# Optimization experiments

Measured on AMD Instinct MI355X. Metric: run time of the kernel, lower is better.

Reference implementation:

```python
import jax, jax.numpy as jnp
import numpy as np

EMBED = 128
HEADS = 8
DH = EMBED // HEADS
FFN_HIDDEN = 512
B, N = 16, 256


def layer_norm(x, g, b, eps=1e-5):
    mu = jnp.mean(x, axis=-1, keepdims=True)
    var = jnp.var(x, axis=-1, keepdims=True)
    return (x - mu) * jax.lax.rsqrt(var + eps) * g + b


def setup_inputs() -> dict:
    key = jax.random.key(0)
    ks = jax.random.split(key, 12)
    s = 1.0 / np.sqrt(EMBED)
    inp = {
        "x": jax.random.normal(ks[0], (B, N, EMBED), jnp.float32),
        "global_rel_pe": jax.random.normal(ks[1], (B, N, N, EMBED), jnp.float32),
        "attn_mask": jnp.zeros((B, N, N), jnp.float32),
        "ln1_g": jnp.ones((EMBED,), jnp.float32),
        "ln1_b": jnp.zeros((EMBED,), jnp.float32),
        "Wq": jax.random.normal(ks[2], (EMBED, EMBED), jnp.float32) * s,
        "bq": jnp.zeros((EMBED,), jnp.float32),
        "Wk": jax.random.normal(ks[3], (EMBED, EMBED), jnp.float32) * s,
        "bk": jnp.zeros((EMBED,), jnp.float32),
        "Wv": jax.random.normal(ks[4], (EMBED, EMBED), jnp.float32) * s,
        "bv": jnp.zeros((EMBED,), jnp.float32),
        "Wo": jax.random.normal(ks[5], (EMBED, EMBED), jnp.float32) * s,
        "bo": jnp.zeros((EMBED,), jnp.float32),
        "ln2_g": jnp.ones((EMBED,), jnp.float32),
        "ln2_b": jnp.zeros((EMBED,), jnp.float32),
        "W1": jax.random.normal(ks[6], (EMBED, FFN_HIDDEN), jnp.float32) * s,
        "b1": jnp.zeros((FFN_HIDDEN,), jnp.float32),
        "W2": jax.random.normal(ks[7], (FFN_HIDDEN, EMBED), jnp.float32) * (1.0 / np.sqrt(FFN_HIDDEN)),
        "b2": jnp.zeros((EMBED,), jnp.float32),
    }
    return inp


def reference(x, global_rel_pe, attn_mask, ln1_g, ln1_b, Wq, bq, Wk, bk, Wv, bv,
              Wo, bo, ln2_g, ln2_b, W1, b1, W2, b2):
    b, n, d = x.shape
    xn = layer_norm(x, ln1_g, ln1_b)
    q = (xn @ Wq + bq).reshape(b, n, HEADS, DH)
    k = (xn @ Wk + bk).reshape(b, n, HEADS, DH)
    v = (xn @ Wv + bv).reshape(b, n, HEADS, DH)
    pe = global_rel_pe.reshape(b, n, n, HEADS, DH)
    # content scores + rel-pos scores: key augmented per-pair by rel_pe
    content = jnp.einsum("bihd,bjhd->bhij", q, k)
    pos = jnp.einsum("bihd,bijhd->bhij", q, pe)
    scores = (content + pos) * (1.0 / np.sqrt(DH)) + attn_mask[:, None]
    attn = jax.nn.softmax(scores, axis=-1)  # [B,H,N,N]
    ctx = jnp.einsum("bhij,bjhd->bihd", attn, v).reshape(b, n, d)
    attn_out = ctx @ Wo + bo
    x = x + attn_out
    xn = layer_norm(x, ln2_g, ln2_b)
    ffn = jax.nn.relu(xn @ W1 + b1) @ W2 + b2
    return x + ffn
```

## Files before the change

### kernel.cpp

```cpp
#include <hip/hip_runtime.h>
#include <hip/hip_bf16.h>
#include <hip/hip_fp16.h>

#define EMBED 128
#define HEADS 8
#define DH 16
#define FFN 512
#define BB 16
#define NN 256

typedef float floatx4 __attribute__((ext_vector_type(4)));

__global__ __launch_bounds__(128) void ln1_qkv_kernel(
    const float* __restrict__ x,
    const float* __restrict__ ln1_g, const float* __restrict__ ln1_b,
    const float* __restrict__ Wq, const float* __restrict__ bq,
    const float* __restrict__ Wk, const float* __restrict__ bk,
    const float* __restrict__ Wv, const float* __restrict__ bv,
    float* __restrict__ q, float* __restrict__ k, float* __restrict__ v)
{
    const int row0 = blockIdx.x * 8;
    const int t    = threadIdx.x;
    const int wv_  = t >> 6;
    const int l64  = t & 63;

    __shared__ float xn[8][EMBED];

    #pragma unroll
    for (int rr = 0; rr < 4; ++rr) {
        const int r = wv_ * 4 + rr;
        const float v0 = x[(size_t)(row0 + r) * EMBED + l64];
        const float v1 = x[(size_t)(row0 + r) * EMBED + 64 + l64];
        float s  = v0 + v1;
        float sq = v0 * v0 + v1 * v1;
        #pragma unroll
        for (int off = 32; off >= 1; off >>= 1) {
            s  += __shfl_xor(s, off);
            sq += __shfl_xor(sq, off);
        }
        const float mu  = s * (1.0f / EMBED);
        const float var = sq * (1.0f / EMBED) - mu * mu;
        const float rs  = rsqrtf(var + 1e-5f);
        xn[r][l64]      = (v0 - mu) * rs * ln1_g[l64]      + ln1_b[l64];
        xn[r][l64 + 64] = (v1 - mu) * rs * ln1_g[l64 + 64] + ln1_b[l64 + 64];
    }
    __syncthreads();

    const int e = t;
    float aq[8], ak[8], av[8];
    const float bqe = bq[e], bke = bk[e], bve = bv[e];
    #pragma unroll
    for (int r = 0; r < 8; ++r) { aq[r] = bqe; ak[r] = bke; av[r] = bve; }

    #pragma unroll 4
    for (int c = 0; c < EMBED; ++c) {
        const float wq = Wq[c * EMBED + e];
        const float wk = Wk[c * EMBED + e];
        const float wv2 = Wv[c * EMBED + e];
        #pragma unroll
        for (int r = 0; r < 8; ++r) {
            const float xc = xn[r][c];
            aq[r] += xc * wq;
            ak[r] += xc * wk;
            av[r] += xc * wv2;
        }
    }
    #pragma unroll
    for (int r = 0; r < 8; ++r) {
        const size_t o = (size_t)(row0 + r) * EMBED + e;
        q[o] = aq[r]; k[o] = ak[r]; v[o] = av[r];
    }
}

__global__ __launch_bounds__(256) void scores_pv_kernel(
    const float* __restrict__ pe,
    const float* __restrict__ mask,
    const float* __restrict__ q, const float* __restrict__ k,
    const float* __restrict__ v,
    const float* __restrict__ x,
    const float* __restrict__ Wo, const float* __restrict__ bo,
    const float* __restrict__ ln2_g, const float* __restrict__ ln2_b,
    float* __restrict__ x2g, float* __restrict__ xn2g)
{
    const int bid  = blockIdx.x;
    const int blk  = (bid & 7) * 128 + (bid >> 3);
    const int row0 = blk * 4;
    const int bb   = row0 >> 8;
    const int t    = threadIdx.x;

    __shared__ __half sc[4][HEADS][264];
    __shared__ float msk[4][NN];
    __shared__ float red4[4][4][EMBED];
    __shared__ float ctx[4][EMBED];
    __shared__ float wred[2][4][EMBED];
    __shared__ float x2s[4][EMBED];

    const int g = t >> 5;
    const int l = t & 31;

    #pragma unroll
    for (int r = 0; r < 4; ++r)
        msk[r][t] = mask[(size_t)(row0 + r) * NN + t];

    floatx4 q4[4];
    #pragma unroll
    for (int r = 0; r < 4; ++r)
        q4[r] = *reinterpret_cast<const floatx4*>(q + (size_t)(row0 + r) * EMBED + 4 * l);

    const size_t pe_base = (size_t)row0 * NN * EMBED;
    const size_t k_row   = (size_t)bb * NN * EMBED;
    const int rot = blk & 31;

    #pragma unroll 4
    for (int jt0 = 0; jt0 < 32; ++jt0) {
        const int jt = (jt0 + rot) & 31;
        const int j  = jt * 8 + g;
        const floatx4 k4 = *reinterpret_cast<const floatx4*>(k + k_row + (size_t)j * EMBED + 4 * l);
        #pragma unroll
        for (int r = 0; r < 4; ++r) {
            const floatx4 p4 = __builtin_nontemporal_load(
                reinterpret_cast<const floatx4*>(pe + pe_base + ((size_t)r * NN + j) * EMBED + 4 * l));
            const floatx4 sum = k4 + p4;
            float s = q4[r].x * sum.x + q4[r].y * sum.y + q4[r].z * sum.z + q4[r].w * sum.w;
            s += __shfl_xor(s, 1);
            s += __shfl_xor(s, 2);
            if ((l & 3) == 0) sc[r][l >> 2][j] = __float2half(s * 0.25f);
        }
    }
    __syncthreads();

    #pragma unroll
    for (int r = 0; r < 4; ++r) {
        float vals[8];
        float m = -1e30f;
        #pragma unroll
        for (int rr = 0; rr < 8; ++rr) {
            vals[rr] = __half2float(sc[r][g][l + 32 * rr]) + msk[r][l + 32 * rr];
            m = fmaxf(m, vals[rr]);
        }
        #pragma unroll
        for (int off = 16; off >= 1; off >>= 1) m = fmaxf(m, __shfl_xor(m, off));
        float ssum = 0.f;
        #pragma unroll
        for (int rr = 0; rr < 8; ++rr) { float e2 = __expf(vals[rr] - m); vals[rr] = e2; ssum += e2; }
        #pragma unroll
        for (int off = 16; off >= 1; off >>= 1) ssum += __shfl_xor(ssum, off);
        const float inv = 1.0f / ssum;
        #pragma unroll
        for (int rr = 0; rr < 8; ++rr) sc[r][g][l + 32 * rr] = __float2half(vals[rr] * inv);
    }
    __syncthreads();

    {
        const int e4  = t & 31;
        const int seg = t >> 5;
        const int h   = e4 >> 2;
        floatx4 acc0 = {0,0,0,0}, acc1 = acc0, acc2 = acc0, acc3 = acc0;
        const float* vb = v + ((size_t)(bb * NN + seg * 32)) * EMBED + 4 * e4;
        #pragma unroll 4
        for (int jj = 0; jj < 32; ++jj) {
            const floatx4 v4 = *reinterpret_cast<const floatx4*>(vb + (size_t)jj * EMBED);
            acc0 += __half2float(sc[0][h][seg * 32 + jj]) * v4;
            acc1 += __half2float(sc[1][h][seg * 32 + jj]) * v4;
            acc2 += __half2float(sc[2][h][seg * 32 + jj]) * v4;
            acc3 += __half2float(sc[3][h][seg * 32 + jj]) * v4;
        }
        acc0.x += __shfl_xor(acc0.x, 32); acc0.y += __shfl_xor(acc0.y, 32);
        acc0.z += __shfl_xor(acc0.z, 32); acc0.w += __shfl_xor(acc0.w, 32);
        acc1.x += __shfl_xor(acc1.x, 32); acc1.y += __shfl_xor(acc1.y, 32);
        acc1.z += __shfl_xor(acc1.z, 32); acc1.w += __shfl_xor(acc1.w, 32);
        acc2.x += __shfl_xor(acc2.x, 32); acc2.y += __shfl_xor(acc2.y, 32);
        acc2.z += __shfl_xor(acc2.z, 32); acc2.w += __shfl_xor(acc2.w, 32);
        acc3.x += __shfl_xor(acc3.x, 32); acc3.y += __shfl_xor(acc3.y, 32);
        acc3.z += __shfl_xor(acc3.z, 32); acc3.w += __shfl_xor(acc3.w, 32);
        if ((t & 63) < 32) {
            const int w = t >> 6;
            *reinterpret_cast<floatx4*>(&red4[w][0][4 * e4]) = acc0;
            *reinterpret_cast<floatx4*>(&red4[w][1][4 * e4]) = acc1;
            *reinterpret_cast<floatx4*>(&red4[w][2][4 * e4]) = acc2;
            *reinterpret_cast<floatx4*>(&red4[w][3][4 * e4]) = acc3;
        }
    }
    __syncthreads();
    {
        #pragma unroll
        for (int rr = 0; rr < 2; ++rr) {
            const int idx = t + 256 * rr;
            const int r = idx >> 7, e = idx & 127;
            ctx[r][e] = red4[0][r][e] + red4[1][r][e] + red4[2][r][e] + red4[3][r][e];
        }
    }
    __syncthreads();

    {
        const int e = t & 127, rp = t >> 7;
        float a0 = 0.f, a1 = 0.f, a2 = 0.f, a3 = 0.f;
        const float* Wob = Wo + rp * 64 * EMBED + e;
        #pragma unroll 8
        for (int cc = 0; cc < 64; ++cc) {
            const float w = Wob[(size_t)cc * EMBED];
            a0 += ctx[0][rp * 64 + cc] * w;
            a1 += ctx[1][rp * 64 + cc] * w;
            a2 += ctx[2][rp * 64 + cc] * w;
            a3 += ctx[3][rp * 64 + cc] * w;
        }
        wred[rp][0][e] = a0; wred[rp][1][e] = a1;
        wred[rp][2][e] = a2; wred[rp][3][e] = a3;
    }
    __syncthreads();

    {
        #pragma unroll
        for (int rr = 0; rr < 2; ++rr) {
            const int idx = t + 256 * rr;
            const int r = idx >> 7, e = idx & 127;
            const float a2 = wred[0][r][e] + wred[1][r][e] + bo[e]
                           + x[(size_t)(row0 + r) * EMBED + e];
            x2s[r][e] = a2;
            x2g[(size_t)(row0 + r) * EMBED + e] = a2;
        }
    }
    __syncthreads();

    {
        const int wid = t >> 6, l64 = t & 63;
        const float v0 = x2s[wid][l64], v1 = x2s[wid][l64 + 64];
        float s  = v0 + v1;
        float sq = v0 * v0 + v1 * v1;
        #pragma unroll
        for (int off = 32; off >= 1; off >>= 1) {
            s  += __shfl_xor(s, off);
            sq += __shfl_xor(sq, off);
        }
        const float mu  = s * (1.0f / EMBED);
        const float var = sq * (1.0f / EMBED) - mu * mu;
        const float rs  = rsqrtf(var + 1e-5f);
        xn2g[(size_t)(row0 + wid) * EMBED + l64] =
            (v0 - mu) * rs * ln2_g[l64] + ln2_b[l64];
        xn2g[(size_t)(row0 + wid) * EMBED + 64 + l64] =
            (v1 - mu) * rs * ln2_g[l64 + 64] + ln2_b[l64 + 64];
    }
}

__global__ __launch_bounds__(512) void ffn_kernel(
    const float* __restrict__ x2g,
    const float* __restrict__ xn2g,
    const float* __restrict__ W1, const float* __restrict__ b1,
    const float* __restrict__ W2, const float* __restrict__ b2,
    float* __restrict__ out)
{
    const int row0 = blockIdx.x * 8;
    const int t    = threadIdx.x;

    __shared__ float xn2s[8][EMBED];
    __shared__ float hb[8][FFN];
    __shared__ float redf[4][8][EMBED];

    if (t < 256) {
        const floatx4 v4 = *reinterpret_cast<const floatx4*>(
            xn2g + (size_t)row0 * EMBED + 4 * t);
        *reinterpret_cast<floatx4*>(&xn2s[0][0] + 4 * t) = v4;
    }
    __syncthreads();

    {
        float h[8];
        const float c0 = b1[t];
        #pragma unroll
        for (int r = 0; r < 8; ++r) h[r] = c0;
        #pragma unroll 4
        for (int c = 0; c < EMBED; ++c) {
            const float w = W1[c * FFN + t];
            #pragma unroll
            for (int r = 0; r < 8; ++r) h[r] += xn2s[r][c] * w;
        }
        #pragma unroll
        for (int r = 0; r < 8; ++r) hb[r][t] = fmaxf(h[r], 0.f);
    }
    __syncthreads();

    {
        const int e = t & 127, qd = t >> 7;
        float a[8];
        #pragma unroll
        for (int r = 0; r < 8; ++r) a[r] = 0.f;
        const float* W2b = W2 + (size_t)(qd * 128) * EMBED + e;
        #pragma unroll 4
        for (int ff = 0; ff < 128; ++ff) {
            const float w = W2b[(size_t)ff * EMBED];
            #pragma unroll
            for (int r = 0; r < 8; ++r) a[r] += hb[r][qd * 128 + ff] * w;
        }
        #pragma unroll
        for (int r = 0; r < 8; ++r) redf[qd][r][e] = a[r];
    }
    __syncthreads();

    {
        #pragma unroll
        for (int rr = 0; rr < 2; ++rr) {
            const int idx = t + 512 * rr;
            const int r = idx >> 7, e = idx & 127;
            out[(size_t)(row0 + r) * EMBED + e] =
                x2g[(size_t)(row0 + r) * EMBED + e] + b2[e]
                + redf[0][r][e] + redf[1][r][e] + redf[2][r][e] + redf[3][r][e];
        }
    }
}

extern "C" void kernel_launch(void* const* d_in, const int* in_sizes, int n_in,
                              void* d_out, int out_size, void* d_ws, size_t ws_size,
                              hipStream_t stream) {
    const float* x    = (const float*)d_in[0];
    const float* pe   = (const float*)d_in[1];
    const float* mask = (const float*)d_in[2];
    const float* ln1g = (const float*)d_in[3];
    const float* ln1b = (const float*)d_in[4];
    const float* Wq   = (const float*)d_in[5];
    const float* bq   = (const float*)d_in[6];
    const float* Wk   = (const float*)d_in[7];
    const float* bk   = (const float*)d_in[8];
    const float* Wv   = (const float*)d_in[9];
    const float* bv   = (const float*)d_in[10];
    const float* Wo   = (const float*)d_in[11];
    const float* bo   = (const float*)d_in[12];
    const float* ln2g = (const float*)d_in[13];
    const float* ln2b = (const float*)d_in[14];
    const float* W1   = (const float*)d_in[15];
    const float* b1   = (const float*)d_in[16];
    const float* W2   = (const float*)d_in[17];
    const float* b2   = (const float*)d_in[18];
    float* out = (float*)d_out;

    float* q    = (float*)d_ws;
    float* kk   = q    + (size_t)BB * NN * EMBED;
    float* vv   = kk   + (size_t)BB * NN * EMBED;
    float* x2g  = vv   + (size_t)BB * NN * EMBED;
    float* xn2g = x2g  + (size_t)BB * NN * EMBED;

    ln1_qkv_kernel<<<BB * NN / 8, 128, 0, stream>>>(x, ln1g, ln1b, Wq, bq, Wk, bk, Wv, bv, q, kk, vv);
    scores_pv_kernel<<<BB * NN / 4, 256, 0, stream>>>(pe, mask, q, kk, vv, x, Wo, bo,
                                                      ln2g, ln2b, x2g, xn2g);
    ffn_kernel<<<BB * NN / 8, 512, 0, stream>>>(x2g, xn2g, W1, b1, W2, b2, out);
}
```

Before: 156.4 us.

## Fuse FFN into the attention kernel, reusing shared memory pools

Folds the FFN (W1, ReLU, W2, residual) into the tail of the scores/PV kernel, so each 4-row block computes its output directly. The separate FFN launch and the global round-trip of x2 and xn2 go away. The score and mask shared buffers are aliased as raw pools for the hidden activations and the normalised rows, so shared usage does not grow. In exchange, each block now reads W1 and W2 for only 4 rows instead of 8, which doubles the total weight traffic, and the FFN work runs inside a kernel that is likely bound by the pe stream.

```diff
diff --git a/kernel.cpp b/kernel.cpp
--- a/kernel.cpp
+++ b/kernel.cpp
@@ -72,7 +72,9 @@
     }
 }
 
-__global__ __launch_bounds__(256) void scores_pv_kernel(
+typedef __half scrow_t[HEADS][264];
+
+__global__ __launch_bounds__(256) void scores_pv_ffn_kernel(
     const float* __restrict__ pe,
     const float* __restrict__ mask,
     const float* __restrict__ q, const float* __restrict__ k,
@@ -80,7 +82,9 @@
     const float* __restrict__ x,
     const float* __restrict__ Wo, const float* __restrict__ bo,
     const float* __restrict__ ln2_g, const float* __restrict__ ln2_b,
-    float* __restrict__ x2g, float* __restrict__ xn2g)
+    const float* __restrict__ W1, const float* __restrict__ b1,
+    const float* __restrict__ W2, const float* __restrict__ b2,
+    float* __restrict__ out)
 {
     const int bid  = blockIdx.x;
     const int blk  = (bid & 7) * 128 + (bid >> 3);
@@ -88,12 +92,17 @@
     const int bb   = row0 >> 8;
     const int t    = threadIdx.x;
 
-    __shared__ __half sc[4][HEADS][264];
-    __shared__ float msk[4][NN];
+    __shared__ __align__(16) unsigned char poolA[4 * sizeof(scrow_t)];
+    __shared__ __align__(16) unsigned char poolB[4 * NN * 4];
     __shared__ float red4[4][4][EMBED];
     __shared__ float ctx[4][EMBED];
     __shared__ float wred[2][4][EMBED];
     __shared__ float x2s[4][EMBED];
+
+    scrow_t* sc = reinterpret_cast<scrow_t*>(poolA);
+    float (*hb)[FFN] = reinterpret_cast<float (*)[FFN]>(poolA);
+    float (*msk)[NN] = reinterpret_cast<float (*)[NN]>(poolB);
+    float (*xn2)[EMBED] = reinterpret_cast<float (*)[EMBED]>(poolB);
 
     const int g = t >> 5;
     const int l = t & 31;
@@ -214,10 +223,8 @@
         for (int rr = 0; rr < 2; ++rr) {
             const int idx = t + 256 * rr;
             const int r = idx >> 7, e = idx & 127;
-            const float a2 = wred[0][r][e] + wred[1][r][e] + bo[e]
-                           + x[(size_t)(row0 + r) * EMBED + e];
-            x2s[r][e] = a2;
-            x2g[(size_t)(row0 + r) * EMBED + e] = a2;
+            x2s[r][e] = wred[0][r][e] + wred[1][r][e] + bo[e]
+                      + x[(size_t)(row0 + r) * EMBED + e];
         }
     }
     __syncthreads();
@@ -235,75 +242,59 @@
         const float mu  = s * (1.0f / EMBED);
         const float var = sq * (1.0f / EMBED) - mu * mu;
         const float rs  = rsqrtf(var + 1e-5f);
-        xn2g[(size_t)(row0 + wid) * EMBED + l64] =
-            (v0 - mu) * rs * ln2_g[l64] + ln2_b[l64];
-        xn2g[(size_t)(row0 + wid) * EMBED + 64 + l64] =
-            (v1 - mu) * rs * ln2_g[l64 + 64] + ln2_b[l64 + 64];
-    }
-}
-
-__global__ __launch_bounds__(512) void ffn_kernel(
-    const float* __restrict__ x2g,
-    const float* __restrict__ xn2g,
-    const float* __restrict__ W1, const float* __restrict__ b1,
-    const float* __restrict__ W2, const float* __restrict__ b2,
-    float* __restrict__ out)
-{
-    const int row0 = blockIdx.x * 8;
-    const int t    = threadIdx.x;
-
-    __shared__ float xn2s[8][EMBED];
-    __shared__ float hb[8][FFN];
-    __shared__ float redf[4][8][EMBED];
-
-    if (t < 256) {
-        const floatx4 v4 = *reinterpret_cast<const floatx4*>(
-            xn2g + (size_t)row0 * EMBED + 4 * t);
-        *reinterpret_cast<floatx4*>(&xn2s[0][0] + 4 * t) = v4;
-    }
-    __syncthreads();
-
-    {
-        float h[8];
-        const float c0 = b1[t];
-        #pragma unroll
-        for (int r = 0; r < 8; ++r) h[r] = c0;
+        xn2[wid][l64]      = (v0 - mu) * rs * ln2_g[l64]      + ln2_b[l64];
+        xn2[wid][l64 + 64] = (v1 - mu) * rs * ln2_g[l64 + 64] + ln2_b[l64 + 64];
+    }
+    __syncthreads();
+
+    {
+        float h0[4], h1[4];
+        const float c0 = b1[t], c1 = b1[t + 256];
+        #pragma unroll
+        for (int r = 0; r < 4; ++r) { h0[r] = c0; h1[r] = c1; }
         #pragma unroll 4
         for (int c = 0; c < EMBED; ++c) {
-            const float w = W1[c * FFN + t];
+            const float w0 = W1[c * FFN + t];
+            const float w1 = W1[c * FFN + t + 256];
             #pragma unroll
-            for (int r = 0; r < 8; ++r) h[r] += xn2s[r][c] * w;
-        }
-        #pragma unroll
-        for (int r = 0; r < 8; ++r) hb[r][t] = fmaxf(h[r], 0.f);
-    }
-    __syncthreads();
-
-    {
-        const int e = t & 127, qd = t >> 7;
-        float a[8];
-        #pragma unroll
-        for (int r = 0; r < 8; ++r) a[r] = 0.f;
-        const float* W2b = W2 + (size_t)(qd * 128) * EMBED + e;
-        #pragma unroll 4
-        for (int ff = 0; ff < 128; ++ff) {
+            for (int r = 0; r < 4; ++r) {
+                const float xc = xn2[r][c];
+                h0[r] += xc * w0;
+                h1[r] += xc * w1;
+            }
+        }
+        #pragma unroll
+        for (int r = 0; r < 4; ++r) {
+            hb[r][t]       = fmaxf(h0[r], 0.f);
+            hb[r][t + 256] = fmaxf(h1[r], 0.f);
+        }
+    }
+    __syncthreads();
+
+    {
+        const int e = t & 127, rp = t >> 7;
+        float a0 = 0.f, a1 = 0.f, a2 = 0.f, a3 = 0.f;
+        const float* W2b = W2 + (size_t)(rp * 256) * EMBED + e;
+        #pragma unroll 8
+        for (int ff = 0; ff < 256; ++ff) {
             const float w = W2b[(size_t)ff * EMBED];
-            #pragma unroll
-            for (int r = 0; r < 8; ++r) a[r] += hb[r][qd * 128 + ff] * w;
-        }
-        #pragma unroll
-        for (int r = 0; r < 8; ++r) redf[qd][r][e] = a[r];
+            a0 += hb[0][rp * 256 + ff] * w;
+            a1 += hb[1][rp * 256 + ff] * w;
+            a2 += hb[2][rp * 256 + ff] * w;
+            a3 += hb[3][rp * 256 + ff] * w;
+        }
+        wred[rp][0][e] = a0; wred[rp][1][e] = a1;
+        wred[rp][2][e] = a2; wred[rp][3][e] = a3;
     }
     __syncthreads();
 
     {
         #pragma unroll
         for (int rr = 0; rr < 2; ++rr) {
-            const int idx = t + 512 * rr;
+            const int idx = t + 256 * rr;
             const int r = idx >> 7, e = idx & 127;
             out[(size_t)(row0 + r) * EMBED + e] =
-                x2g[(size_t)(row0 + r) * EMBED + e] + b2[e]
-                + redf[0][r][e] + redf[1][r][e] + redf[2][r][e] + redf[3][r][e];
+                x2s[r][e] + b2[e] + wred[0][r][e] + wred[1][r][e];
         }
     }
 }
@@ -332,14 +323,12 @@
     const float* b2   = (const float*)d_in[18];
     float* out = (float*)d_out;
 
-    float* q    = (float*)d_ws;
-    float* kk   = q    + (size_t)BB * NN * EMBED;
-    float* vv   = kk   + (size_t)BB * NN * EMBED;
-    float* x2g  = vv   + (size_t)BB * NN * EMBED;
-    float* xn2g = x2g  + (size_t)BB * NN * EMBED;
+    float* q  = (float*)d_ws;
+    float* kk = q  + (size_t)BB * NN * EMBED;
+    float* vv = kk + (size_t)BB * NN * EMBED;
 
     ln1_qkv_kernel<<<BB * NN / 8, 128, 0, stream>>>(x, ln1g, ln1b, Wq, bq, Wk, bk, Wv, bv, q, kk, vv);
-    scores_pv_kernel<<<BB * NN / 4, 256, 0, stream>>>(pe, mask, q, kk, vv, x, Wo, bo,
-                                                      ln2g, ln2b, x2g, xn2g);
-    ffn_kernel<<<BB * NN / 8, 512, 0, stream>>>(x2g, xn2g, W1, b1, W2, b2, out);
+    scores_pv_ffn_kernel<<<BB * NN / 4, 256, 0, stream>>>(pe, mask, q, kk, vv, x,
+                                                          Wo, bo, ln2g, ln2b,
+                                                          W1, b1, W2, b2, out);
 }
```

New measurement: 153.1 us. 2.1% less time.
